# Performance work log

Measured on AMD Instinct MI355X. Metric: run time of the kernel, lower is better.

Reference implementation:

```python
import jax, jax.numpy as jnp
import numpy as np

N = 131072      # packets
KD = 128        # key_dim
DM = 256        # d_model
HD = 256        # hidden_dim
NC = 1024       # num_compute_nodes
AD = 64         # address_dim
SCALE = 0.1     # residual_scale
ROLE_WRITER = 0


def _ln(x, g, b, eps=1e-5):
    m = jnp.mean(x, axis=-1, keepdims=True)
    v = jnp.mean((x - m) ** 2, axis=-1, keepdims=True)
    return (x - m) * jax.lax.rsqrt(v + eps) * g + b


def setup_inputs() -> dict:
    key = jax.random.key(0)
    ks = jax.random.split(key, 16)
    f32 = jnp.float32

    def w(k, shape):
        return jax.random.normal(k, shape, dtype=f32) * 0.02

    inp = {
        "routing_key": jax.random.normal(ks[0], (N, KD), f32),
        "aux_features": jax.random.normal(ks[1], (N, DM), f32),
        "residual": jax.random.normal(ks[2], (N, DM), f32),
        "role": jax.random.randint(ks[3], (N,), 0, 3, dtype=jnp.int32),
        # input projections
        "Wk": w(ks[4], (KD, HD)), "bk": jnp.zeros((HD,), f32),
        "Wa": w(ks[5], (DM, HD)), "ba": jnp.zeros((HD,), f32),
        "Wr": w(ks[6], (DM, HD)), "br": jnp.zeros((HD,), f32),
        # input layernorm
        "g_in": jnp.ones((HD,), f32), "b_in": jnp.zeros((HD,), f32),
        # backbone layer 0 (Linear + GELU + LN)
        "Wb0": w(ks[7], (HD, HD)), "bb0": jnp.zeros((HD,), f32),
        "g0": jnp.ones((HD,), f32), "beta0": jnp.zeros((HD,), f32),
        # backbone layer 1
        "Wb1": w(ks[8], (HD, HD)), "bb1": jnp.zeros((HD,), f32),
        "g1": jnp.ones((HD,), f32), "beta1": jnp.zeros((HD,), f32),
        # role-specific heads
        "Ww": w(ks[9], (HD, NC)), "bw": jnp.zeros((NC,), f32),
        "Wq": w(ks[10], (HD, NC)), "bq": jnp.zeros((NC,), f32),
        # address head (aux_type == 'address_l2')
        "Wad": w(ks[11], (HD, AD)), "bad": jnp.zeros((AD,), f32),
    }
    return inp


def reference(routing_key, aux_features, residual, role,
              Wk, bk, Wa, ba, Wr, br, g_in, b_in,
              Wb0, bb0, g0, beta0, Wb1, bb1, g1, beta1,
              Ww, bw, Wq, bq, Wad, bad):
    # hidden = key_proj(key) + aux_proj(aux) + scale * residual_proj(residual)
    h = (routing_key @ Wk + bk) + (aux_features @ Wa + ba) \
        + SCALE * (residual @ Wr + br)
    h = _ln(h, g_in, b_in)
    # backbone: [Linear -> GELU -> LN] x layers
    for W, bL, g, be in ((Wb0, bb0, g0, beta0), (Wb1, bb1, g1, beta1)):
        h = _ln(jax.nn.gelu(h @ W + bL, approximate=False), g, be)
    # role-masked head dispatch: writers use writer_head; query + other rows
    # use query_head (matches the torch masked gather/scatter semantics)
    writer = (role == ROLE_WRITER)[:, None]
    logits = jnp.where(writer, h @ Ww + bw, h @ Wq + bq)
    aux_address = h @ Wad + bad
    return logits, h, aux_address
```

## Files before the change

kernel.cpp:

```cpp
#include <hip/hip_runtime.h>
#include <hip/hip_bf16.h>

#define N_PKT 131072
#define KD 128
#define DM 256
#define HDIM 256
#define NCOMP 1024
#define ADIM 64

typedef __attribute__((ext_vector_type(8))) short v8s;
typedef __attribute__((ext_vector_type(4))) float v4f;

__device__ inline unsigned short f2bf(float f) {
  __hip_bfloat16 h = __float2bfloat16(f);
  return *reinterpret_cast<unsigned short*>(&h);
}

__device__ inline float bf2f(unsigned short u) {
  return __uint_as_float(((unsigned)u) << 16);
}

__device__ inline float gelu_f(float x) {
  float x2 = x * x;
  float p = fmaf(x2, 0.10294540f, 2.30208889f);
  float e = __builtin_amdgcn_exp2f(x * p);
  float r = __builtin_amdgcn_rcpf(1.0f + e);
  return x - x * r;
}

struct PrepParams {
  const float *Wk, *Wa, *Wr, *Wb0, *Wb1, *Ww, *Wq, *Wad;
  const float *bk, *ba, *br, *bb0, *bb1;
  const float *g_in, *b_in, *g0, *be0;
  unsigned short* P;
  float* bcomb; float* bb0adj; float* bb1adj;
};

__global__ void prep_kern(PrepParams pp) {
  const int tid = threadIdx.x;
  if (blockIdx.x >= 3264) {
    if (blockIdx.x == 3264) {
      pp.bcomb[tid] = pp.bk[tid] + pp.ba[tid] + 0.1f * pp.br[tid];
    } else {
      const float* vsrc = (blockIdx.x == 3265) ? pp.b_in : pp.be0;
      const float* Wsrc = (blockIdx.x == 3265) ? pp.Wb0 : pp.Wb1;
      const float* badd = (blockIdx.x == 3265) ? pp.bb0 : pp.bb1;
      float* dst = (blockIdx.x == 3265) ? pp.bb0adj : pp.bb1adj;
      float s = badd[tid];
      #pragma unroll 8
      for (int k = 0; k < 256; ++k) s = fmaf(vsrc[k], Wsrc[(long)k * 256 + tid], s);
      dst[tid] = s;
    }
    return;
  }
  long gid = (long)blockIdx.x * 256 + tid;
  int K, Nc; long base; int seg;
  if      (gid < 163840) { K = 640; Nc = 256;  base = 0;      seg = 0; }
  else if (gid < 229376) { K = 256; Nc = 256;  base = 163840; seg = 1; }
  else if (gid < 294912) { K = 256; Nc = 256;  base = 229376; seg = 2; }
  else if (gid < 557056) { K = 256; Nc = 1024; base = 294912; seg = 3; }
  else if (gid < 819200) { K = 256; Nc = 1024; base = 557056; seg = 4; }
  else                   { K = 256; Nc = 64;   base = 819200; seg = 5; }
  long idx = gid - base;
  int j = (int)(idx & 7);
  int l = (int)((idx >> 3) & 63);
  long t = idx >> 9;
  int nKT = K >> 5;
  int kt = (int)(t % nKT), nt = (int)(t / nKT);
  int k = kt * 32 + (l >> 4) * 8 + j;
  int n = nt * 16 + (l & 15);
  float v;
  if (seg == 0) {
    if (k < 128)      v = pp.Wk[(long)k * 256 + n];
    else if (k < 384) v = pp.Wa[(long)(k - 128) * 256 + n];
    else              v = 0.1f * pp.Wr[(long)(k - 384) * 256 + n];
  } else if (seg == 1) v = pp.g_in[k] * pp.Wb0[(long)k * 256 + n];
  else if (seg == 2)   v = pp.g0[k] * pp.Wb1[(long)k * 256 + n];
  else if (seg == 3)   v = pp.Ww[(long)k * Nc + n];
  else if (seg == 4)   v = pp.Wq[(long)k * Nc + n];
  else                 v = pp.Wad[(long)k * Nc + n];
  pp.P[gid] = f2bf(v);
}

template<int COLS>
__device__ inline void stage_tile(const float* __restrict__ src, long R0,
                                  unsigned short (&tile)[64][264], int tid) {
  constexpr int C4 = COLS / 4;
  constexpr int NV = 64 * C4;
  #pragma unroll
  for (int i = 0; i < NV / 256; ++i) {
    int idx = tid + i * 256;
    int r = idx / C4;
    int c4 = idx % C4;
    float4 v = *(reinterpret_cast<const float4*>(src + (R0 + r) * (long)COLS) + c4);
    unsigned long long pk = (unsigned long long)f2bf(v.x)
                          | ((unsigned long long)f2bf(v.y) << 16)
                          | ((unsigned long long)f2bf(v.z) << 32)
                          | ((unsigned long long)f2bf(v.w) << 48);
    *reinterpret_cast<unsigned long long*>(&tile[r][c4 * 4]) = pk;
  }
}

template<int NKT, int KTOFF, int KSTRIDE>
__device__ inline void gemm_acc(const unsigned short* __restrict__ Wp, int nt0,
                                const unsigned short (&tile)[64][264], int lane,
                                v4f (&acc)[4][4]) {
  const int lr = lane & 15, lg = lane >> 4;
  #pragma unroll
  for (int kt = 0; kt < NKT; ++kt) {
    v8s b[4];
    #pragma unroll
    for (int nf = 0; nf < 4; ++nf)
      b[nf] = *reinterpret_cast<const v8s*>(
          Wp + (((long)(nt0 + nf) * KSTRIDE + KTOFF + kt) * 64 + lane) * 8);
    #pragma unroll
    for (int m = 0; m < 4; ++m) {
      v8s a = *reinterpret_cast<const v8s*>(&tile[m * 16 + lr][kt * 32 + lg * 8]);
      #pragma unroll
      for (int nf = 0; nf < 4; ++nf)
        acc[m][nf] = __builtin_amdgcn_mfma_f32_16x16x32_bf16(a, b[nf], acc[m][nf], 0, 0, 0);
    }
  }
}

__device__ inline void init_acc(v4f (&acc)[4][4], const float* __restrict__ bias,
                                int colbase, int lr) {
  float bv[4];
  #pragma unroll
  for (int nf = 0; nf < 4; ++nf) bv[nf] = bias[colbase + nf * 16 + lr];
  #pragma unroll
  for (int m = 0; m < 4; ++m)
    #pragma unroll
    for (int nf = 0; nf < 4; ++nf)
      acc[m][nf] = (v4f){bv[nf], bv[nf], bv[nf], bv[nf]};
}

template<bool GELU, bool AFFINE>
__device__ inline void ln_stage(v4f (&acc)[4][4], int wave, int lane,
                                const float* __restrict__ gamma, const float* __restrict__ beta,
                                unsigned short (&tile)[64][264], float (&stats)[2][4][64]) {
  const int lr = lane & 15, lg = lane >> 4;
  if (GELU) {
    #pragma unroll
    for (int m = 0; m < 4; ++m)
      #pragma unroll
      for (int nf = 0; nf < 4; ++nf)
        #pragma unroll
        for (int r = 0; r < 4; ++r)
          acc[m][nf][r] = gelu_f(acc[m][nf][r]);
  }
  float s[4][4], q[4][4];
  #pragma unroll
  for (int m = 0; m < 4; ++m)
    #pragma unroll
    for (int r = 0; r < 4; ++r) {
      float t = 0.f, t2 = 0.f;
      #pragma unroll
      for (int nf = 0; nf < 4; ++nf) { float v = acc[m][nf][r]; t += v; t2 = fmaf(v, v, t2); }
      s[m][r] = t; q[m][r] = t2;
    }
  #pragma unroll
  for (int off = 1; off < 16; off <<= 1)
    #pragma unroll
    for (int m = 0; m < 4; ++m)
      #pragma unroll
      for (int r = 0; r < 4; ++r) {
        s[m][r] += __shfl_xor(s[m][r], off);
        q[m][r] += __shfl_xor(q[m][r], off);
      }
  if (lr == 0) {
    #pragma unroll
    for (int m = 0; m < 4; ++m)
      #pragma unroll
      for (int r = 0; r < 4; ++r) {
        int row = m * 16 + lg * 4 + r;
        stats[0][wave][row] = s[m][r];
        stats[1][wave][row] = q[m][r];
      }
  }
  __syncthreads();
  float gv[4], bv[4];
  if (AFFINE) {
    #pragma unroll
    for (int nf = 0; nf < 4; ++nf) {
      int c = wave * 64 + nf * 16 + lr;
      gv[nf] = gamma[c]; bv[nf] = beta[c];
    }
  }
  #pragma unroll
  for (int m = 0; m < 4; ++m)
    #pragma unroll
    for (int r = 0; r < 4; ++r) {
      int row = m * 16 + lg * 4 + r;
      float S = stats[0][0][row] + stats[0][1][row] + stats[0][2][row] + stats[0][3][row];
      float Q = stats[1][0][row] + stats[1][1][row] + stats[1][2][row] + stats[1][3][row];
      float mean = S * (1.0f / 256.0f);
      float var  = Q * (1.0f / 256.0f) - mean * mean;
      float rstd = rsqrtf(var + 1e-5f);
      #pragma unroll
      for (int nf = 0; nf < 4; ++nf) {
        int c = wave * 64 + nf * 16 + lr;
        float z = (acc[m][nf][r] - mean) * rstd;
        float y = AFFINE ? fmaf(z, gv[nf], bv[nf]) : z;
        tile[row][c] = f2bf(y);
      }
    }
  __syncthreads();
}

struct MegaParams {
  const float* key; const float* aux; const float* res; const int* role;
  const unsigned short* pWcat; const unsigned short* pWb0; const unsigned short* pWb1;
  const unsigned short* pWad; const unsigned short* pWw; const unsigned short* pWq;
  const float* bcomb; const float* bb0adj; const float* bb1adj;
  const float* g1; const float* be1; const float* bad;
  const float* bw; const float* bq;
  float* out_logits; float* out_h; float* out_aux;
};

__global__ __launch_bounds__(256, 3) void mega_kern(MegaParams p) {
  __shared__ alignas(16) unsigned short tile[64][264];
  __shared__ float stats[2][4][64];
  __shared__ alignas(16) float stage[4][16][68];
  __shared__ unsigned char wf[64];

  const int tid = threadIdx.x;
  const int lane = tid & 63;
  const int wave = tid >> 6;
  const int lr = lane & 15;
  const int lg = lane >> 4;
  const long R0 = (long)blockIdx.x * 64;
  const int nt0 = wave * 4;

  if (tid < 64) wf[tid] = (p.role[R0 + tid] == 0) ? 1 : 0;

  v4f acc[4][4];

  init_acc(acc, p.bcomb, wave * 64, lr);
  stage_tile<KD>(p.key, R0, tile, tid);
  __syncthreads();
  gemm_acc<4, 0, 20>(p.pWcat, nt0, tile, lane, acc);
  __syncthreads();
  stage_tile<DM>(p.aux, R0, tile, tid);
  __syncthreads();
  gemm_acc<8, 4, 20>(p.pWcat, nt0, tile, lane, acc);
  __syncthreads();
  stage_tile<DM>(p.res, R0, tile, tid);
  __syncthreads();
  gemm_acc<8, 12, 20>(p.pWcat, nt0, tile, lane, acc);
  ln_stage<false, false>(acc, wave, lane, nullptr, nullptr, tile, stats);

  init_acc(acc, p.bb0adj, wave * 64, lr);
  gemm_acc<8, 0, 8>(p.pWb0, nt0, tile, lane, acc);
  ln_stage<true, false>(acc, wave, lane, nullptr, nullptr, tile, stats);

  init_acc(acc, p.bb1adj, wave * 64, lr);
  gemm_acc<8, 0, 8>(p.pWb1, nt0, tile, lane, acc);
  ln_stage<true, true>(acc, wave, lane, p.g1, p.be1, tile, stats);

  #pragma unroll
  for (int i = 0; i < 16; ++i) {
    int row = wave * 16 + i;
    unsigned long long t4 = *reinterpret_cast<const unsigned long long*>(&tile[row][lane * 4]);
    v4f v;
    v[0] = bf2f((unsigned short)(t4 & 0xffff));
    v[1] = bf2f((unsigned short)((t4 >> 16) & 0xffff));
    v[2] = bf2f((unsigned short)((t4 >> 32) & 0xffff));
    v[3] = bf2f((unsigned short)((t4 >> 48) & 0xffff));
    *reinterpret_cast<v4f*>(p.out_h + (R0 + row) * HDIM + lane * 4) = v;
  }

  {
    float (*astage)[68] = reinterpret_cast<float(*)[68]>(&stage[0][0][0]);
    v4f a4[4];
    float bv = p.bad[wave * 16 + lr];
    #pragma unroll
    for (int m = 0; m < 4; ++m) a4[m] = (v4f){bv, bv, bv, bv};
    #pragma unroll
    for (int kt = 0; kt < 8; ++kt) {
      v8s b = *reinterpret_cast<const v8s*>(p.pWad + (((long)wave * 8 + kt) * 64 + lane) * 8);
      #pragma unroll
      for (int m = 0; m < 4; ++m) {
        v8s am = *reinterpret_cast<const v8s*>(&tile[m * 16 + lr][kt * 32 + lg * 8]);
        a4[m] = __builtin_amdgcn_mfma_f32_16x16x32_bf16(am, b, a4[m], 0, 0, 0);
      }
    }
    #pragma unroll
    for (int m = 0; m < 4; ++m)
      #pragma unroll
      for (int r = 0; r < 4; ++r)
        astage[m * 16 + lg * 4 + r][wave * 16 + lr] = a4[m][r];
    __syncthreads();
    #pragma unroll
    for (int k = 0; k < 4; ++k) {
      int idx = tid + k * 256;
      int row = idx >> 4;
      int c4 = idx & 15;
      v4f v = *reinterpret_cast<const v4f*>(&astage[row][c4 * 4]);
      *reinterpret_cast<v4f*>(p.out_aux + (R0 + row) * ADIM + c4 * 4) = v;
    }
    __syncthreads();
  }

  const int rr = lane >> 3;
  const int ce = lane & 7;
  #pragma unroll 1
  for (int hsel = 0; hsel < 2; ++hsel) {
    const unsigned short* Wp = hsel == 0 ? p.pWw : p.pWq;
    const float* bias = hsel == 0 ? p.bw : p.bq;
    const unsigned char want = hsel == 0 ? 1 : 0;
    #pragma unroll 1
    for (int c = 0; c < 4; ++c) {
      const int nth = wave * 16 + c * 4;
      v4f hacc[4][4];
      #pragma unroll
      for (int nf = 0; nf < 4; ++nf) {
        v4f bv = *reinterpret_cast<const v4f*>(bias + (nth + nf) * 16 + lg * 4);
        #pragma unroll
        for (int m = 0; m < 4; ++m) hacc[m][nf] = bv;
      }
      v8s wcur[4], wnxt[4];
      #pragma unroll
      for (int nf = 0; nf < 4; ++nf)
        wcur[nf] = *reinterpret_cast<const v8s*>(Wp + (((long)(nth + nf) * 8 + 0) * 64 + lane) * 8);
      #pragma unroll
      for (int kt = 0; kt < 8; ++kt) {
        if (kt < 7) {
          #pragma unroll
          for (int nf = 0; nf < 4; ++nf)
            wnxt[nf] = *reinterpret_cast<const v8s*>(Wp + (((long)(nth + nf) * 8 + kt + 1) * 64 + lane) * 8);
        }
        #pragma unroll
        for (int m = 0; m < 4; ++m) {
          v8s a = *reinterpret_cast<const v8s*>(&tile[m * 16 + lr][kt * 32 + lg * 8]);
          #pragma unroll
          for (int nf = 0; nf < 4; ++nf)
            hacc[m][nf] = __builtin_amdgcn_mfma_f32_16x16x32_bf16(wcur[nf], a, hacc[m][nf], 0, 0, 0);
        }
        if (kt < 7) {
          #pragma unroll
          for (int nf = 0; nf < 4; ++nf) wcur[nf] = wnxt[nf];
        }
      }
      #pragma unroll
      for (int m = 0; m < 4; ++m) {
        #pragma unroll
        for (int nf = 0; nf < 4; ++nf)
          *reinterpret_cast<v4f*>(&stage[wave][lr][nf * 16 + lg * 4]) = hacc[m][nf];
        __builtin_amdgcn_sched_barrier(0);
        #pragma unroll
        for (int rh = 0; rh < 2; ++rh) {
          int row = m * 16 + rh * 8 + rr;
          bool doit = (wf[row] == want);
          #pragma unroll
          for (int ch = 0; ch < 2; ++ch) {
            v4f v = *reinterpret_cast<const v4f*>(&stage[wave][rh * 8 + rr][ch * 32 + ce * 4]);
            if (doit)
              *reinterpret_cast<v4f*>(p.out_logits + (R0 + row) * NCOMP
                                      + nth * 16 + ch * 32 + ce * 4) = v;
          }
        }
        __builtin_amdgcn_sched_barrier(0);
      }
    }
  }
}

extern "C" void kernel_launch(void* const* d_in, const int* in_sizes, int n_in,
                              void* d_out, int out_size, void* d_ws, size_t ws_size,
                              hipStream_t stream) {
  const float* key  = (const float*)d_in[0];
  const float* aux  = (const float*)d_in[1];
  const float* res  = (const float*)d_in[2];
  const int*   role = (const int*)d_in[3];
  const float* Wk = (const float*)d_in[4];   const float* bk = (const float*)d_in[5];
  const float* Wa = (const float*)d_in[6];   const float* ba = (const float*)d_in[7];
  const float* Wr = (const float*)d_in[8];   const float* br = (const float*)d_in[9];
  const float* g_in = (const float*)d_in[10]; const float* b_in = (const float*)d_in[11];
  const float* Wb0 = (const float*)d_in[12]; const float* bb0 = (const float*)d_in[13];
  const float* g0 = (const float*)d_in[14];  const float* be0 = (const float*)d_in[15];
  const float* Wb1 = (const float*)d_in[16]; const float* bb1 = (const float*)d_in[17];
  const float* g1 = (const float*)d_in[18];  const float* be1 = (const float*)d_in[19];
  const float* Ww = (const float*)d_in[20];  const float* bw = (const float*)d_in[21];
  const float* Wq = (const float*)d_in[22];  const float* bq = (const float*)d_in[23];
  const float* Wad = (const float*)d_in[24]; const float* bad = (const float*)d_in[25];

  unsigned short* wsp = (unsigned short*)d_ws;
  unsigned short* pWcat = wsp + 0;
  unsigned short* pWb0  = wsp + 163840;
  unsigned short* pWb1  = wsp + 229376;
  unsigned short* pWw   = wsp + 294912;
  unsigned short* pWq   = wsp + 557056;
  unsigned short* pWad  = wsp + 819200;
  char* wsb = (char*)d_ws;
  float* bcomb  = (float*)(wsb + 1671168);
  float* bb0adj = (float*)(wsb + 1672192);
  float* bb1adj = (float*)(wsb + 1673216);

  PrepParams pp;
  pp.Wk = Wk; pp.Wa = Wa; pp.Wr = Wr; pp.Wb0 = Wb0; pp.Wb1 = Wb1;
  pp.Ww = Ww; pp.Wq = Wq; pp.Wad = Wad;
  pp.bk = bk; pp.ba = ba; pp.br = br; pp.bb0 = bb0; pp.bb1 = bb1;
  pp.g_in = g_in; pp.b_in = b_in; pp.g0 = g0; pp.be0 = be0;
  pp.P = wsp; pp.bcomb = bcomb; pp.bb0adj = bb0adj; pp.bb1adj = bb1adj;
  prep_kern<<<3267, 256, 0, stream>>>(pp);

  float* out = (float*)d_out;
  MegaParams P;
  P.key = key; P.aux = aux; P.res = res; P.role = role;
  P.pWcat = pWcat; P.pWb0 = pWb0; P.pWb1 = pWb1; P.pWad = pWad;
  P.pWw = pWw; P.pWq = pWq;
  P.bcomb = bcomb; P.bb0adj = bb0adj; P.bb1adj = bb1adj;
  P.g1 = g1; P.be1 = be1; P.bad = bad; P.bw = bw; P.bq = bq;
  P.out_logits = out;
  P.out_h = out + (size_t)N_PKT * NCOMP;
  P.out_aux = out + (size_t)N_PKT * (NCOMP + HDIM);
  mega_kern<<<N_PKT / 64, 256, 0, stream>>>(P);
}
```

Baseline: 410.6 us.

## Compact rows by role and compute only the matching head per tile

Adds a stream-compaction pass that splits packet indices into writer and non-writer lists. The mega kernel then processes 64-row tiles drawn from one list, gathers the input rows by index, and computes only the one head (Ww or Wq) that applies, instead of computing both heads and masking the stores. This roughly halves the head GEMM work. In exchange it adds gathered loads, scattered stores, atomics, two extra small launches and padded tiles.

Measured after the change: 451.7 us. 1.1x slower.

```diff
diff --git a/kernel.cpp b/kernel.cpp
--- a/kernel.cpp
+++ b/kernel.cpp
@@ -34,6 +34,7 @@
   const float *g_in, *b_in, *g0, *be0;
   unsigned short* P;
   float* bcomb; float* bb0adj; float* bb1adj;
+  int* cnt;
 };
 
 __global__ void prep_kern(PrepParams pp) {
@@ -41,6 +42,7 @@
   if (blockIdx.x >= 3264) {
     if (blockIdx.x == 3264) {
       pp.bcomb[tid] = pp.bk[tid] + pp.ba[tid] + 0.1f * pp.br[tid];
+      if (tid < 2) pp.cnt[tid] = 0;
     } else {
       const float* vsrc = (blockIdx.x == 3265) ? pp.b_in : pp.be0;
       const float* Wsrc = (blockIdx.x == 3265) ? pp.Wb0 : pp.Wb1;
@@ -82,21 +84,56 @@
   pp.P[gid] = f2bf(v);
 }
 
+__global__ void compact_kern(const int* __restrict__ role, int* __restrict__ wIdx,
+                             int* __restrict__ qIdx, int* __restrict__ cnt) {
+  int r = blockIdx.x * 256 + threadIdx.x;
+  int lane = threadIdx.x & 63;
+  bool w = (role[r] == 0);
+  unsigned long long mw = __ballot(w);
+  unsigned long long below = (lane == 0) ? 0ull : (~0ull >> (64 - lane));
+  int pw = __popcll(mw & below);
+  int cw = __popcll(mw);
+  int base = 0;
+  if (lane == 0) base = atomicAdd(&cnt[0], cw);
+  base = __shfl(base, 0);
+  if (w) wIdx[base + pw] = r;
+  unsigned long long mq = ~mw;
+  int pq = __popcll(mq & below);
+  int cq = 64 - cw;
+  int baseq = 0;
+  if (lane == 0) baseq = atomicAdd(&cnt[1], cq);
+  baseq = __shfl(baseq, 0);
+  if (!w) qIdx[baseq + pq] = r;
+}
+
+__global__ void finalize_kern(const int* __restrict__ cnt, int* __restrict__ wIdx,
+                              int* __restrict__ qIdx, int* __restrict__ meta) {
+  int cw = cnt[0], cq = cnt[1];
+  int nwT = (cw + 63) >> 6, nqT = (cq + 63) >> 6;
+  int tid = threadIdx.x;
+  for (int i = cw + tid; i < nwT * 64; i += 64) wIdx[i] = -1;
+  for (int i = cq + tid; i < nqT * 64; i += 64) qIdx[i] = -1;
+  if (tid == 0) { meta[0] = nwT; meta[1] = nqT; }
+}
+
 template<int COLS>
-__device__ inline void stage_tile(const float* __restrict__ src, long R0,
-                                  unsigned short (&tile)[64][264], int tid) {
+__device__ inline void gather_stage(const float* __restrict__ src, const int* rows,
+                                    unsigned short (&tile)[64][264], int tid) {
   constexpr int C4 = COLS / 4;
-  constexpr int NV = 64 * C4;
-  #pragma unroll
-  for (int i = 0; i < NV / 256; ++i) {
+  #pragma unroll
+  for (int i = 0; i < 64 * C4 / 256; ++i) {
     int idx = tid + i * 256;
     int r = idx / C4;
     int c4 = idx % C4;
-    float4 v = *(reinterpret_cast<const float4*>(src + (R0 + r) * (long)COLS) + c4);
-    unsigned long long pk = (unsigned long long)f2bf(v.x)
-                          | ((unsigned long long)f2bf(v.y) << 16)
-                          | ((unsigned long long)f2bf(v.z) << 32)
-                          | ((unsigned long long)f2bf(v.w) << 48);
+    int ridx = rows[r];
+    unsigned long long pk = 0ull;
+    if (ridx >= 0) {
+      float4 v = *(reinterpret_cast<const float4*>(src + (long)ridx * COLS) + c4);
+      pk = (unsigned long long)f2bf(v.x)
+         | ((unsigned long long)f2bf(v.y) << 16)
+         | ((unsigned long long)f2bf(v.z) << 32)
+         | ((unsigned long long)f2bf(v.w) << 48);
+    }
     *reinterpret_cast<unsigned long long*>(&tile[r][c4 * 4]) = pk;
   }
 }
@@ -209,12 +246,13 @@
 }
 
 struct MegaParams {
-  const float* key; const float* aux; const float* res; const int* role;
+  const float* key; const float* aux; const float* res;
   const unsigned short* pWcat; const unsigned short* pWb0; const unsigned short* pWb1;
   const unsigned short* pWad; const unsigned short* pWw; const unsigned short* pWq;
   const float* bcomb; const float* bb0adj; const float* bb1adj;
   const float* g1; const float* be1; const float* bad;
   const float* bw; const float* bq;
+  const int* wIdx; const int* qIdx; const int* meta;
   float* out_logits; float* out_h; float* out_aux;
 };
 
@@ -222,30 +260,36 @@
   __shared__ alignas(16) unsigned short tile[64][264];
   __shared__ float stats[2][4][64];
   __shared__ alignas(16) float stage[4][16][68];
-  __shared__ unsigned char wf[64];
+  __shared__ int rows[64];
+
+  const int t = blockIdx.x;
+  const int nwT = p.meta[0], nqT = p.meta[1];
+  if (t >= nwT + nqT) return;
+  const bool isW = (t < nwT);
+  const int* list = isW ? (p.wIdx + (long)t * 64) : (p.qIdx + (long)(t - nwT) * 64);
 
   const int tid = threadIdx.x;
   const int lane = tid & 63;
   const int wave = tid >> 6;
   const int lr = lane & 15;
   const int lg = lane >> 4;
-  const long R0 = (long)blockIdx.x * 64;
   const int nt0 = wave * 4;
 
-  if (tid < 64) wf[tid] = (p.role[R0 + tid] == 0) ? 1 : 0;
+  if (tid < 64) rows[tid] = list[tid];
+  __syncthreads();
 
   v4f acc[4][4];
 
   init_acc(acc, p.bcomb, wave * 64, lr);
-  stage_tile<KD>(p.key, R0, tile, tid);
+  gather_stage<KD>(p.key, rows, tile, tid);
   __syncthreads();
   gemm_acc<4, 0, 20>(p.pWcat, nt0, tile, lane, acc);
   __syncthreads();
-  stage_tile<DM>(p.aux, R0, tile, tid);
+  gather_stage<DM>(p.aux, rows, tile, tid);
   __syncthreads();
   gemm_acc<8, 4, 20>(p.pWcat, nt0, tile, lane, acc);
   __syncthreads();
-  stage_tile<DM>(p.res, R0, tile, tid);
+  gather_stage<DM>(p.res, rows, tile, tid);
   __syncthreads();
   gemm_acc<8, 12, 20>(p.pWcat, nt0, tile, lane, acc);
   ln_stage<false, false>(acc, wave, lane, nullptr, nullptr, tile, stats);
@@ -261,13 +305,15 @@
   #pragma unroll
   for (int i = 0; i < 16; ++i) {
     int row = wave * 16 + i;
+    int ridx = rows[row];
     unsigned long long t4 = *reinterpret_cast<const unsigned long long*>(&tile[row][lane * 4]);
     v4f v;
     v[0] = bf2f((unsigned short)(t4 & 0xffff));
     v[1] = bf2f((unsigned short)((t4 >> 16) & 0xffff));
     v[2] = bf2f((unsigned short)((t4 >> 32) & 0xffff));
     v[3] = bf2f((unsigned short)((t4 >> 48) & 0xffff));
-    *reinterpret_cast<v4f*>(p.out_h + (R0 + row) * HDIM + lane * 4) = v;
+    if (ridx >= 0)
+      *reinterpret_cast<v4f*>(p.out_h + (long)ridx * HDIM + lane * 4) = v;
   }
 
   {
@@ -296,72 +342,69 @@
       int idx = tid + k * 256;
       int row = idx >> 4;
       int c4 = idx & 15;
+      int ridx = rows[row];
       v4f v = *reinterpret_cast<const v4f*>(&astage[row][c4 * 4]);
-      *reinterpret_cast<v4f*>(p.out_aux + (R0 + row) * ADIM + c4 * 4) = v;
+      if (ridx >= 0)
+        *reinterpret_cast<v4f*>(p.out_aux + (long)ridx * ADIM + c4 * 4) = v;
     }
     __syncthreads();
   }
 
+  const unsigned short* Wp = isW ? p.pWw : p.pWq;
+  const float* bias = isW ? p.bw : p.bq;
   const int rr = lane >> 3;
   const int ce = lane & 7;
   #pragma unroll 1
-  for (int hsel = 0; hsel < 2; ++hsel) {
-    const unsigned short* Wp = hsel == 0 ? p.pWw : p.pWq;
-    const float* bias = hsel == 0 ? p.bw : p.bq;
-    const unsigned char want = hsel == 0 ? 1 : 0;
-    #pragma unroll 1
-    for (int c = 0; c < 4; ++c) {
-      const int nth = wave * 16 + c * 4;
-      v4f hacc[4][4];
-      #pragma unroll
-      for (int nf = 0; nf < 4; ++nf) {
-        v4f bv = *reinterpret_cast<const v4f*>(bias + (nth + nf) * 16 + lg * 4);
-        #pragma unroll
-        for (int m = 0; m < 4; ++m) hacc[m][nf] = bv;
-      }
-      v8s wcur[4], wnxt[4];
-      #pragma unroll
-      for (int nf = 0; nf < 4; ++nf)
-        wcur[nf] = *reinterpret_cast<const v8s*>(Wp + (((long)(nth + nf) * 8 + 0) * 64 + lane) * 8);
-      #pragma unroll
-      for (int kt = 0; kt < 8; ++kt) {
-        if (kt < 7) {
-          #pragma unroll
-          for (int nf = 0; nf < 4; ++nf)
-            wnxt[nf] = *reinterpret_cast<const v8s*>(Wp + (((long)(nth + nf) * 8 + kt + 1) * 64 + lane) * 8);
-        }
-        #pragma unroll
-        for (int m = 0; m < 4; ++m) {
-          v8s a = *reinterpret_cast<const v8s*>(&tile[m * 16 + lr][kt * 32 + lg * 8]);
-          #pragma unroll
-          for (int nf = 0; nf < 4; ++nf)
-            hacc[m][nf] = __builtin_amdgcn_mfma_f32_16x16x32_bf16(wcur[nf], a, hacc[m][nf], 0, 0, 0);
-        }
-        if (kt < 7) {
-          #pragma unroll
-          for (int nf = 0; nf < 4; ++nf) wcur[nf] = wnxt[nf];
-        }
-      }
-      #pragma unroll
-      for (int m = 0; m < 4; ++m) {
+  for (int c = 0; c < 4; ++c) {
+    const int nth = wave * 16 + c * 4;
+    v4f hacc[4][4];
+    #pragma unroll
+    for (int nf = 0; nf < 4; ++nf) {
+      v4f bv = *reinterpret_cast<const v4f*>(bias + (nth + nf) * 16 + lg * 4);
+      #pragma unroll
+      for (int m = 0; m < 4; ++m) hacc[m][nf] = bv;
+    }
+    v8s wcur[4], wnxt[4];
+    #pragma unroll
+    for (int nf = 0; nf < 4; ++nf)
+      wcur[nf] = *reinterpret_cast<const v8s*>(Wp + (((long)(nth + nf) * 8 + 0) * 64 + lane) * 8);
+    #pragma unroll
+    for (int kt = 0; kt < 8; ++kt) {
+      if (kt < 7) {
         #pragma unroll
         for (int nf = 0; nf < 4; ++nf)
-          *reinterpret_cast<v4f*>(&stage[wave][lr][nf * 16 + lg * 4]) = hacc[m][nf];
-        __builtin_amdgcn_sched_barrier(0);
+          wnxt[nf] = *reinterpret_cast<const v8s*>(Wp + (((long)(nth + nf) * 8 + kt + 1) * 64 + lane) * 8);
+      }
+      #pragma unroll
+      for (int m = 0; m < 4; ++m) {
+        v8s a = *reinterpret_cast<const v8s*>(&tile[m * 16 + lr][kt * 32 + lg * 8]);
         #pragma unroll
-        for (int rh = 0; rh < 2; ++rh) {
-          int row = m * 16 + rh * 8 + rr;
-          bool doit = (wf[row] == want);
-          #pragma unroll
-          for (int ch = 0; ch < 2; ++ch) {
-            v4f v = *reinterpret_cast<const v4f*>(&stage[wave][rh * 8 + rr][ch * 32 + ce * 4]);
-            if (doit)
-              *reinterpret_cast<v4f*>(p.out_logits + (R0 + row) * NCOMP
-                                      + nth * 16 + ch * 32 + ce * 4) = v;
-          }
+        for (int nf = 0; nf < 4; ++nf)
+          hacc[m][nf] = __builtin_amdgcn_mfma_f32_16x16x32_bf16(wcur[nf], a, hacc[m][nf], 0, 0, 0);
+      }
+      if (kt < 7) {
+        #pragma unroll
+        for (int nf = 0; nf < 4; ++nf) wcur[nf] = wnxt[nf];
+      }
+    }
+    #pragma unroll
+    for (int m = 0; m < 4; ++m) {
+      #pragma unroll
+      for (int nf = 0; nf < 4; ++nf)
+        *reinterpret_cast<v4f*>(&stage[wave][lr][nf * 16 + lg * 4]) = hacc[m][nf];
+      __builtin_amdgcn_sched_barrier(0);
+      #pragma unroll
+      for (int rh = 0; rh < 2; ++rh) {
+        int ridx = rows[m * 16 + rh * 8 + rr];
+        #pragma unroll
+        for (int ch = 0; ch < 2; ++ch) {
+          v4f v = *reinterpret_cast<const v4f*>(&stage[wave][rh * 8 + rr][ch * 32 + ce * 4]);
+          if (ridx >= 0)
+            *reinterpret_cast<v4f*>(p.out_logits + (long)ridx * NCOMP
+                                    + nth * 16 + ch * 32 + ce * 4) = v;
         }
-        __builtin_amdgcn_sched_barrier(0);
-      }
+      }
+      __builtin_amdgcn_sched_barrier(0);
     }
   }
 }
@@ -396,6 +439,10 @@
   float* bcomb  = (float*)(wsb + 1671168);
   float* bb0adj = (float*)(wsb + 1672192);
   float* bb1adj = (float*)(wsb + 1673216);
+  int* wIdx = (int*)(wsb + 1674240);
+  int* qIdx = (int*)(wsb + 2198784);
+  int* cnt  = (int*)(wsb + 2723328);
+  int* meta = (int*)(wsb + 2723336);
 
   PrepParams pp;
   pp.Wk = Wk; pp.Wa = Wa; pp.Wr = Wr; pp.Wb0 = Wb0; pp.Wb1 = Wb1;
@@ -403,17 +450,22 @@
   pp.bk = bk; pp.ba = ba; pp.br = br; pp.bb0 = bb0; pp.bb1 = bb1;
   pp.g_in = g_in; pp.b_in = b_in; pp.g0 = g0; pp.be0 = be0;
   pp.P = wsp; pp.bcomb = bcomb; pp.bb0adj = bb0adj; pp.bb1adj = bb1adj;
+  pp.cnt = cnt;
   prep_kern<<<3267, 256, 0, stream>>>(pp);
+
+  compact_kern<<<N_PKT / 256, 256, 0, stream>>>(role, wIdx, qIdx, cnt);
+  finalize_kern<<<1, 64, 0, stream>>>(cnt, wIdx, qIdx, meta);
 
   float* out = (float*)d_out;
   MegaParams P;
-  P.key = key; P.aux = aux; P.res = res; P.role = role;
+  P.key = key; P.aux = aux; P.res = res;
   P.pWcat = pWcat; P.pWb0 = pWb0; P.pWb1 = pWb1; P.pWad = pWad;
   P.pWw = pWw; P.pWq = pWq;
   P.bcomb = bcomb; P.bb0adj = bb0adj; P.bb1adj = bb1adj;
   P.g1 = g1; P.be1 = be1; P.bad = bad; P.bw = bw; P.bq = bq;
+  P.wIdx = wIdx; P.qIdx = qIdx; P.meta = meta;
   P.out_logits = out;
   P.out_h = out + (size_t)N_PKT * NCOMP;
   P.out_aux = out + (size_t)N_PKT * (NCOMP + HDIM);
-  mega_kern<<<N_PKT / 64, 256, 0, stream>>>(P);
-}
+  mega_kern<<<N_PKT / 64 + 2, 256, 0, stream>>>(P);
+}
```

## Use 512-thread blocks with 8 waves splitting each GEMM's columns

Applied to the files above, without the earlier changes.

Doubles the block to 8 waves over the same 64-row tile. Each wave now owns 32 hidden columns in the backbone GEMMs and half as many head column chunks. LayerNorm statistics are reduced across 8 waves, and only 4 waves compute the address head. The aim is more latency hiding and less per-wave serial work, at the cost of more block-wide barriers, more cross-wave reduction, and lower MFMA reuse per B-fragment load.

Result: slower. 483.9 us (+17.9%).

```diff
diff --git a/kernel.cpp b/kernel.cpp
--- a/kernel.cpp
+++ b/kernel.cpp
@@ -7,6 +7,7 @@
 #define HDIM 256
 #define NCOMP 1024
 #define ADIM 64
+#define TPB 512
 
 typedef __attribute__((ext_vector_type(8))) short v8s;
 typedef __attribute__((ext_vector_type(4))) float v4f;
@@ -88,8 +89,8 @@
   constexpr int C4 = COLS / 4;
   constexpr int NV = 64 * C4;
   #pragma unroll
-  for (int i = 0; i < NV / 256; ++i) {
-    int idx = tid + i * 256;
+  for (int i = 0; i < NV / TPB; ++i) {
+    int idx = tid + i * TPB;
     int r = idx / C4;
     int c4 = idx % C4;
     float4 v = *(reinterpret_cast<const float4*>(src + (R0 + r) * (long)COLS) + c4);
@@ -102,49 +103,48 @@
 }
 
 template<int NKT, int KTOFF, int KSTRIDE>
-__device__ inline void gemm_acc(const unsigned short* __restrict__ Wp, int nt0,
-                                const unsigned short (&tile)[64][264], int lane,
-                                v4f (&acc)[4][4]) {
+__device__ inline void gemm_acc2(const unsigned short* __restrict__ Wp, int nt0,
+                                 const unsigned short (&tile)[64][264], int lane,
+                                 v4f (&acc)[4][2]) {
   const int lr = lane & 15, lg = lane >> 4;
   #pragma unroll
   for (int kt = 0; kt < NKT; ++kt) {
-    v8s b[4];
-    #pragma unroll
-    for (int nf = 0; nf < 4; ++nf)
+    v8s b[2];
+    #pragma unroll
+    for (int nf = 0; nf < 2; ++nf)
       b[nf] = *reinterpret_cast<const v8s*>(
           Wp + (((long)(nt0 + nf) * KSTRIDE + KTOFF + kt) * 64 + lane) * 8);
     #pragma unroll
     for (int m = 0; m < 4; ++m) {
       v8s a = *reinterpret_cast<const v8s*>(&tile[m * 16 + lr][kt * 32 + lg * 8]);
       #pragma unroll
-      for (int nf = 0; nf < 4; ++nf)
+      for (int nf = 0; nf < 2; ++nf)
         acc[m][nf] = __builtin_amdgcn_mfma_f32_16x16x32_bf16(a, b[nf], acc[m][nf], 0, 0, 0);
     }
   }
 }
 
-__device__ inline void init_acc(v4f (&acc)[4][4], const float* __restrict__ bias,
-                                int colbase, int lr) {
-  float bv[4];
-  #pragma unroll
-  for (int nf = 0; nf < 4; ++nf) bv[nf] = bias[colbase + nf * 16 + lr];
-  #pragma unroll
-  for (int m = 0; m < 4; ++m)
-    #pragma unroll
-    for (int nf = 0; nf < 4; ++nf)
-      acc[m][nf] = (v4f){bv[nf], bv[nf], bv[nf], bv[nf]};
+__device__ inline void init_acc2(v4f (&acc)[4][2], const float* __restrict__ bias,
+                                 int colbase, int lr) {
+  #pragma unroll
+  for (int nf = 0; nf < 2; ++nf) {
+    float bv = bias[colbase + nf * 16 + lr];
+    #pragma unroll
+    for (int m = 0; m < 4; ++m)
+      acc[m][nf] = (v4f){bv, bv, bv, bv};
+  }
 }
 
 template<bool GELU, bool AFFINE>
-__device__ inline void ln_stage(v4f (&acc)[4][4], int wave, int lane,
+__device__ inline void ln_stage(v4f (&acc)[4][2], int wave, int lane,
                                 const float* __restrict__ gamma, const float* __restrict__ beta,
-                                unsigned short (&tile)[64][264], float (&stats)[2][4][64]) {
+                                unsigned short (&tile)[64][264], float (&stats)[2][8][64]) {
   const int lr = lane & 15, lg = lane >> 4;
   if (GELU) {
     #pragma unroll
     for (int m = 0; m < 4; ++m)
       #pragma unroll
-      for (int nf = 0; nf < 4; ++nf)
+      for (int nf = 0; nf < 2; ++nf)
         #pragma unroll
         for (int r = 0; r < 4; ++r)
           acc[m][nf][r] = gelu_f(acc[m][nf][r]);
@@ -156,7 +156,7 @@
     for (int r = 0; r < 4; ++r) {
       float t = 0.f, t2 = 0.f;
       #pragma unroll
-      for (int nf = 0; nf < 4; ++nf) { float v = acc[m][nf][r]; t += v; t2 = fmaf(v, v, t2); }
+      for (int nf = 0; nf < 2; ++nf) { float v = acc[m][nf][r]; t += v; t2 = fmaf(v, v, t2); }
       s[m][r] = t; q[m][r] = t2;
     }
   #pragma unroll
@@ -179,11 +179,11 @@
       }
   }
   __syncthreads();
-  float gv[4], bv[4];
+  float gv[2], bv[2];
   if (AFFINE) {
     #pragma unroll
-    for (int nf = 0; nf < 4; ++nf) {
-      int c = wave * 64 + nf * 16 + lr;
+    for (int nf = 0; nf < 2; ++nf) {
+      int c = wave * 32 + nf * 16 + lr;
       gv[nf] = gamma[c]; bv[nf] = beta[c];
     }
   }
@@ -192,14 +192,15 @@
     #pragma unroll
     for (int r = 0; r < 4; ++r) {
       int row = m * 16 + lg * 4 + r;
-      float S = stats[0][0][row] + stats[0][1][row] + stats[0][2][row] + stats[0][3][row];
-      float Q = stats[1][0][row] + stats[1][1][row] + stats[1][2][row] + stats[1][3][row];
+      float S = 0.f, Q = 0.f;
+      #pragma unroll
+      for (int w = 0; w < 8; ++w) { S += stats[0][w][row]; Q += stats[1][w][row]; }
       float mean = S * (1.0f / 256.0f);
       float var  = Q * (1.0f / 256.0f) - mean * mean;
       float rstd = rsqrtf(var + 1e-5f);
       #pragma unroll
-      for (int nf = 0; nf < 4; ++nf) {
-        int c = wave * 64 + nf * 16 + lr;
+      for (int nf = 0; nf < 2; ++nf) {
+        int c = wave * 32 + nf * 16 + lr;
         float z = (acc[m][nf][r] - mean) * rstd;
         float y = AFFINE ? fmaf(z, gv[nf], bv[nf]) : z;
         tile[row][c] = f2bf(y);
@@ -218,10 +219,10 @@
   float* out_logits; float* out_h; float* out_aux;
 };
 
-__global__ __launch_bounds__(256, 3) void mega_kern(MegaParams p) {
+__global__ __launch_bounds__(512, 4) void mega_kern(MegaParams p) {
   __shared__ alignas(16) unsigned short tile[64][264];
-  __shared__ float stats[2][4][64];
-  __shared__ alignas(16) float stage[4][16][68];
+  __shared__ float stats[2][8][64];
+  __shared__ alignas(16) float stage[8][16][68];
   __shared__ unsigned char wf[64];
 
   const int tid = threadIdx.x;
@@ -230,37 +231,37 @@
   const int lr = lane & 15;
   const int lg = lane >> 4;
   const long R0 = (long)blockIdx.x * 64;
-  const int nt0 = wave * 4;
+  const int nt0 = wave * 2;
 
   if (tid < 64) wf[tid] = (p.role[R0 + tid] == 0) ? 1 : 0;
 
-  v4f acc[4][4];
-
-  init_acc(acc, p.bcomb, wave * 64, lr);
+  v4f acc[4][2];
+
+  init_acc2(acc, p.bcomb, wave * 32, lr);
   stage_tile<KD>(p.key, R0, tile, tid);
   __syncthreads();
-  gemm_acc<4, 0, 20>(p.pWcat, nt0, tile, lane, acc);
+  gemm_acc2<4, 0, 20>(p.pWcat, nt0, tile, lane, acc);
   __syncthreads();
   stage_tile<DM>(p.aux, R0, tile, tid);
   __syncthreads();
-  gemm_acc<8, 4, 20>(p.pWcat, nt0, tile, lane, acc);
+  gemm_acc2<8, 4, 20>(p.pWcat, nt0, tile, lane, acc);
   __syncthreads();
   stage_tile<DM>(p.res, R0, tile, tid);
   __syncthreads();
-  gemm_acc<8, 12, 20>(p.pWcat, nt0, tile, lane, acc);
+  gemm_acc2<8, 12, 20>(p.pWcat, nt0, tile, lane, acc);
   ln_stage<false, false>(acc, wave, lane, nullptr, nullptr, tile, stats);
 
-  init_acc(acc, p.bb0adj, wave * 64, lr);
-  gemm_acc<8, 0, 8>(p.pWb0, nt0, tile, lane, acc);
+  init_acc2(acc, p.bb0adj, wave * 32, lr);
+  gemm_acc2<8, 0, 8>(p.pWb0, nt0, tile, lane, acc);
   ln_stage<true, false>(acc, wave, lane, nullptr, nullptr, tile, stats);
 
-  init_acc(acc, p.bb1adj, wave * 64, lr);
-  gemm_acc<8, 0, 8>(p.pWb1, nt0, tile, lane, acc);
+  init_acc2(acc, p.bb1adj, wave * 32, lr);
+  gemm_acc2<8, 0, 8>(p.pWb1, nt0, tile, lane, acc);
   ln_stage<true, true>(acc, wave, lane, p.g1, p.be1, tile, stats);
 
   #pragma unroll
-  for (int i = 0; i < 16; ++i) {
-    int row = wave * 16 + i;
+  for (int i = 0; i < 8; ++i) {
+    int row = wave * 8 + i;
     unsigned long long t4 = *reinterpret_cast<const unsigned long long*>(&tile[row][lane * 4]);
     v4f v;
     v[0] = bf2f((unsigned short)(t4 & 0xffff));
@@ -272,28 +273,30 @@
 
   {
     float (*astage)[68] = reinterpret_cast<float(*)[68]>(&stage[0][0][0]);
-    v4f a4[4];
-    float bv = p.bad[wave * 16 + lr];
-    #pragma unroll
-    for (int m = 0; m < 4; ++m) a4[m] = (v4f){bv, bv, bv, bv};
-    #pragma unroll
-    for (int kt = 0; kt < 8; ++kt) {
-      v8s b = *reinterpret_cast<const v8s*>(p.pWad + (((long)wave * 8 + kt) * 64 + lane) * 8);
-      #pragma unroll
-      for (int m = 0; m < 4; ++m) {
-        v8s am = *reinterpret_cast<const v8s*>(&tile[m * 16 + lr][kt * 32 + lg * 8]);
-        a4[m] = __builtin_amdgcn_mfma_f32_16x16x32_bf16(am, b, a4[m], 0, 0, 0);
-      }
-    }
-    #pragma unroll
-    for (int m = 0; m < 4; ++m)
-      #pragma unroll
-      for (int r = 0; r < 4; ++r)
-        astage[m * 16 + lg * 4 + r][wave * 16 + lr] = a4[m][r];
+    if (wave < 4) {
+      v4f a4[4];
+      float bv = p.bad[wave * 16 + lr];
+      #pragma unroll
+      for (int m = 0; m < 4; ++m) a4[m] = (v4f){bv, bv, bv, bv};
+      #pragma unroll
+      for (int kt = 0; kt < 8; ++kt) {
+        v8s b = *reinterpret_cast<const v8s*>(p.pWad + (((long)wave * 8 + kt) * 64 + lane) * 8);
+        #pragma unroll
+        for (int m = 0; m < 4; ++m) {
+          v8s am = *reinterpret_cast<const v8s*>(&tile[m * 16 + lr][kt * 32 + lg * 8]);
+          a4[m] = __builtin_amdgcn_mfma_f32_16x16x32_bf16(am, b, a4[m], 0, 0, 0);
+        }
+      }
+      #pragma unroll
+      for (int m = 0; m < 4; ++m)
+        #pragma unroll
+        for (int r = 0; r < 4; ++r)
+          astage[m * 16 + lg * 4 + r][wave * 16 + lr] = a4[m][r];
+    }
     __syncthreads();
     #pragma unroll
-    for (int k = 0; k < 4; ++k) {
-      int idx = tid + k * 256;
+    for (int k = 0; k < 2; ++k) {
+      int idx = tid + k * TPB;
       int row = idx >> 4;
       int c4 = idx & 15;
       v4f v = *reinterpret_cast<const v4f*>(&astage[row][c4 * 4]);
@@ -310,8 +313,8 @@
     const float* bias = hsel == 0 ? p.bw : p.bq;
     const unsigned char want = hsel == 0 ? 1 : 0;
     #pragma unroll 1
-    for (int c = 0; c < 4; ++c) {
-      const int nth = wave * 16 + c * 4;
+    for (int c = 0; c < 2; ++c) {
+      const int nth = wave * 8 + c * 4;
       v4f hacc[4][4];
       #pragma unroll
       for (int nf = 0; nf < 4; ++nf) {
@@ -415,5 +418,5 @@
   P.out_logits = out;
   P.out_h = out + (size_t)N_PKT * NCOMP;
   P.out_aux = out + (size_t)N_PKT * (NCOMP + HDIM);
-  mega_kern<<<N_PKT / 64, 256, 0, stream>>>(P);
-}
+  mega_kern<<<N_PKT / 64, TPB, 0, stream>>>(P);
+}
```

## Sort rows by role within tile to skip unused head MFMA blocks

Applied to the files above, without the earlier changes.

Each 64-row block now builds a permutation that puts writer rows first and others after, using a wave ballot and popcount. Inputs are gathered through this permutation, and outputs are scattered back to their original rows. In the head phase, 16-row m-slices that hold no rows for the current head are skipped, which removes much of the redundant compute of evaluating both heads on every row. With random roles only about one or two of the four slices per head can be skipped, and the gathered loads and scattered stores become less regular.

Result: faster. 360.8 us (median of 2 runs) (-12.1%).

```diff
diff --git a/kernel.cpp b/kernel.cpp
--- a/kernel.cpp
+++ b/kernel.cpp
@@ -84,6 +84,7 @@
 
 template<int COLS>
 __device__ inline void stage_tile(const float* __restrict__ src, long R0,
+                                  const int* __restrict__ rows,
                                   unsigned short (&tile)[64][264], int tid) {
   constexpr int C4 = COLS / 4;
   constexpr int NV = 64 * C4;
@@ -92,7 +93,7 @@
     int idx = tid + i * 256;
     int r = idx / C4;
     int c4 = idx % C4;
-    float4 v = *(reinterpret_cast<const float4*>(src + (R0 + r) * (long)COLS) + c4);
+    float4 v = *(reinterpret_cast<const float4*>(src + (R0 + rows[r]) * (long)COLS) + c4);
     unsigned long long pk = (unsigned long long)f2bf(v.x)
                           | ((unsigned long long)f2bf(v.y) << 16)
                           | ((unsigned long long)f2bf(v.z) << 32)
@@ -222,7 +223,8 @@
   __shared__ alignas(16) unsigned short tile[64][264];
   __shared__ float stats[2][4][64];
   __shared__ alignas(16) float stage[4][16][68];
-  __shared__ unsigned char wf[64];
+  __shared__ int rows[64];
+  __shared__ int nwS;
 
   const int tid = threadIdx.x;
   const int lane = tid & 63;
@@ -232,20 +234,30 @@
   const long R0 = (long)blockIdx.x * 64;
   const int nt0 = wave * 4;
 
-  if (tid < 64) wf[tid] = (p.role[R0 + tid] == 0) ? 1 : 0;
+  if (tid < 64) {
+    int w = (p.role[R0 + tid] == 0) ? 1 : 0;
+    unsigned long long mw = __ballot(w != 0);
+    unsigned long long below = (tid == 0) ? 0ull : (~0ull >> (64 - tid));
+    int nw = __popcll(mw);
+    int pos = w ? __popcll(mw & below) : nw + __popcll((~mw) & below);
+    rows[pos] = tid;
+    if (tid == 0) nwS = nw;
+  }
+  __syncthreads();
+  const int nw = nwS;
 
   v4f acc[4][4];
 
   init_acc(acc, p.bcomb, wave * 64, lr);
-  stage_tile<KD>(p.key, R0, tile, tid);
+  stage_tile<KD>(p.key, R0, rows, tile, tid);
   __syncthreads();
   gemm_acc<4, 0, 20>(p.pWcat, nt0, tile, lane, acc);
   __syncthreads();
-  stage_tile<DM>(p.aux, R0, tile, tid);
+  stage_tile<DM>(p.aux, R0, rows, tile, tid);
   __syncthreads();
   gemm_acc<8, 4, 20>(p.pWcat, nt0, tile, lane, acc);
   __syncthreads();
-  stage_tile<DM>(p.res, R0, tile, tid);
+  stage_tile<DM>(p.res, R0, rows, tile, tid);
   __syncthreads();
   gemm_acc<8, 12, 20>(p.pWcat, nt0, tile, lane, acc);
   ln_stage<false, false>(acc, wave, lane, nullptr, nullptr, tile, stats);
@@ -260,14 +272,14 @@
 
   #pragma unroll
   for (int i = 0; i < 16; ++i) {
-    int row = wave * 16 + i;
-    unsigned long long t4 = *reinterpret_cast<const unsigned long long*>(&tile[row][lane * 4]);
+    int slot = wave * 16 + i;
+    unsigned long long t4 = *reinterpret_cast<const unsigned long long*>(&tile[slot][lane * 4]);
     v4f v;
     v[0] = bf2f((unsigned short)(t4 & 0xffff));
     v[1] = bf2f((unsigned short)((t4 >> 16) & 0xffff));
     v[2] = bf2f((unsigned short)((t4 >> 32) & 0xffff));
     v[3] = bf2f((unsigned short)((t4 >> 48) & 0xffff));
-    *reinterpret_cast<v4f*>(p.out_h + (R0 + row) * HDIM + lane * 4) = v;
+    *reinterpret_cast<v4f*>(p.out_h + (R0 + rows[slot]) * HDIM + lane * 4) = v;
   }
 
   {
@@ -294,10 +306,10 @@
     #pragma unroll
     for (int k = 0; k < 4; ++k) {
       int idx = tid + k * 256;
-      int row = idx >> 4;
+      int slot = idx >> 4;
       int c4 = idx & 15;
-      v4f v = *reinterpret_cast<const v4f*>(&astage[row][c4 * 4]);
-      *reinterpret_cast<v4f*>(p.out_aux + (R0 + row) * ADIM + c4 * 4) = v;
+      v4f v = *reinterpret_cast<const v4f*>(&astage[slot][c4 * 4]);
+      *reinterpret_cast<v4f*>(p.out_aux + (R0 + rows[slot]) * ADIM + c4 * 4) = v;
     }
     __syncthreads();
   }
@@ -308,7 +320,10 @@
   for (int hsel = 0; hsel < 2; ++hsel) {
     const unsigned short* Wp = hsel == 0 ? p.pWw : p.pWq;
     const float* bias = hsel == 0 ? p.bw : p.bq;
-    const unsigned char want = hsel == 0 ? 1 : 0;
+    bool needm[4];
+    #pragma unroll
+    for (int m = 0; m < 4; ++m)
+      needm[m] = (hsel == 0) ? (m * 16 < nw) : ((m + 1) * 16 > nw);
     #pragma unroll 1
     for (int c = 0; c < 4; ++c) {
       const int nth = wave * 16 + c * 4;
@@ -332,6 +347,7 @@
         }
         #pragma unroll
         for (int m = 0; m < 4; ++m) {
+          if (!needm[m]) continue;
           v8s a = *reinterpret_cast<const v8s*>(&tile[m * 16 + lr][kt * 32 + lg * 8]);
           #pragma unroll
           for (int nf = 0; nf < 4; ++nf)
@@ -344,19 +360,21 @@
       }
       #pragma unroll
       for (int m = 0; m < 4; ++m) {
+        if (!needm[m]) continue;
         #pragma unroll
         for (int nf = 0; nf < 4; ++nf)
           *reinterpret_cast<v4f*>(&stage[wave][lr][nf * 16 + lg * 4]) = hacc[m][nf];
         __builtin_amdgcn_sched_barrier(0);
         #pragma unroll
         for (int rh = 0; rh < 2; ++rh) {
-          int row = m * 16 + rh * 8 + rr;
-          bool doit = (wf[row] == want);
+          int slot = m * 16 + rh * 8 + rr;
+          bool doit = (hsel == 0) ? (slot < nw) : (slot >= nw);
+          int ridx = rows[slot];
           #pragma unroll
           for (int ch = 0; ch < 2; ++ch) {
             v4f v = *reinterpret_cast<const v4f*>(&stage[wave][rh * 8 + rr][ch * 32 + ce * 4]);
             if (doit)
-              *reinterpret_cast<v4f*>(p.out_logits + (R0 + row) * NCOMP
+              *reinterpret_cast<v4f*>(p.out_logits + (R0 + ridx) * NCOMP
                                       + nth * 16 + ch * 32 + ce * 4) = v;
           }
         }
```
